# Optimization experiments

Hardware: AMD Instinct MI355X
Metric: run time of the kernel (lower is better)

Reference implementation:

```python
import jax, jax.numpy as jnp
import numpy as np

S, B, H = 1024, 2, 1024
NH, NKV, HD = 16, 4, 64
E, TOPK, F = 8, 2, 2048
EPS = 1e-5


def _layer_norm(x, w, b):
    mu = jnp.mean(x, axis=-1, keepdims=True)
    var = jnp.mean(jnp.square(x - mu), axis=-1, keepdims=True)
    return (x - mu) * jax.lax.rsqrt(var + EPS) * w + b


def setup_inputs() -> dict:
    key = jax.random.key(0)
    ks = jax.random.split(key, 8)
    return {
        "hidden_states": jax.random.normal(ks[0], (S, B, H), jnp.float32),
        "ln1_weight": jnp.ones((H,), jnp.float32),
        "ln1_bias": jnp.zeros((H,), jnp.float32),
        "ln2_weight": jnp.ones((H,), jnp.float32),
        "ln2_bias": jnp.zeros((H,), jnp.float32),
        "qkv_weight": jax.random.normal(ks[1], ((NH + 2 * NKV) * HD, H), jnp.float32) * 0.02,
        "proj_weight": jax.random.normal(ks[2], (H, H), jnp.float32) * 0.02,
        "router_weight": jax.random.normal(ks[3], (E, H), jnp.float32) * 0.02,
        "moe_w1": jax.random.normal(ks[4], (E, H, F), jnp.float32) * 0.02,
        "moe_w2": jax.random.normal(ks[5], (E, F, H), jnp.float32) * 0.02,
    }


def reference(hidden_states, ln1_weight, ln1_bias, ln2_weight, ln2_bias,
              qkv_weight, proj_weight, router_weight, moe_w1, moe_w2):
    dtype = hidden_states.dtype
    # LN1 -> QKV projection
    ln1_out = _layer_norm(hidden_states, ln1_weight, ln1_bias)            # [S,B,H]
    qkv = jnp.einsum('sbh,oh->sbo', ln1_out, qkv_weight)                  # [S,B,(NH+2NKV)*HD]
    q = qkv[..., : NH * HD].reshape(S, B, NH, HD)
    k = qkv[..., NH * HD: (NH + NKV) * HD].reshape(S, B, NKV, HD)
    v = qkv[..., (NH + NKV) * HD:].reshape(S, B, NKV, HD)
    # GQA: expand kv heads (repeat_interleave along head dim)
    ratio = NH // NKV
    k = jnp.repeat(k, ratio, axis=2)                                      # [S,B,NH,HD]
    v = jnp.repeat(v, ratio, axis=2)
    # [S,B,h,d] -> [B,h,S,d]
    qb = jnp.transpose(q, (1, 2, 0, 3))
    kb = jnp.transpose(k, (1, 2, 0, 3))
    vb = jnp.transpose(v, (1, 2, 0, 3))
    scale = 1.0 / np.sqrt(HD)
    scores = jnp.einsum('bhqd,bhkd->bhqk', qb, kb) * scale                # [B,NH,S,S]
    causal = jnp.tril(jnp.ones((S, S), bool))
    scores = jnp.where(causal, scores, jnp.finfo(dtype).min)
    attn = jax.nn.softmax(scores, axis=-1)
    attn_out = jnp.einsum('bhqk,bhkd->bhqd', attn, vb)                    # [B,NH,S,HD]
    attn_out = jnp.transpose(attn_out, (2, 0, 1, 3)).reshape(S, B, H)     # [S,B,H]
    proj_out = jnp.einsum('sbh,oh->sbo', attn_out, proj_weight)
    hidden_after_attn = hidden_states + proj_out
    # LN2 -> MoE
    ln2_flat = _layer_norm(hidden_after_attn, ln2_weight, ln2_bias).reshape(-1, H)  # [T,H]
    logits = jnp.einsum('th,eh->te', ln2_flat, router_weight)             # [T,E]
    probs = jax.nn.softmax(logits, axis=-1)
    top_probs, top_idx = jax.lax.top_k(probs, TOPK)                       # [T,K]
    # combine gate: sum_k prob_k * onehot(expert_k)  -> [T,E]
    gate = jnp.sum(jax.nn.one_hot(top_idx, E, dtype=dtype) * top_probs[..., None], axis=1)
    # dense all-expert grouped GEMM equivalent of dispatch/FC1/act/FC2/combine
    h1 = jnp.einsum('th,ehf->tef', ln2_flat, moe_w1)                      # [T,E,F]
    a1 = jax.nn.gelu(h1)
    y = jnp.einsum('tef,efh->teh', a1, moe_w2)                            # [T,E,H]
    moe_out = jnp.einsum('te,teh->th', gate, y).reshape(S, B, H)
    return hidden_after_attn + moe_out
```

## Files before the change

### kernel.cpp

```cpp
#include <hip/hip_runtime.h>
#include <hip/hip_bf16.h>

typedef unsigned short u16;
typedef __attribute__((ext_vector_type(8))) short s16x8;
typedef __attribute__((ext_vector_type(4))) short s16x4;
typedef __attribute__((ext_vector_type(4))) float f32x4;

#define SEQ 1024
#define BATCH 2
#define HID 1024
#define NHEAD 16
#define NKVH 4
#define HDIM 64
#define NEXP 8
#define FFN 2048
#define TOK (SEQ*BATCH)
#define QKVO ((NHEAD + 2*NKVH)*HDIM)
#define NPART 80
#define PREC 2112

#define GL16(gp, lp) __builtin_amdgcn_global_load_lds( \
    (const __attribute__((address_space(1))) unsigned int*)(gp), \
    (__attribute__((address_space(3))) unsigned int*)(lp), 16, 0, 0)

#define WAVE_LDS_FENCE() do { \
    asm volatile("s_waitcnt lgkmcnt(0)" ::: "memory"); \
    __builtin_amdgcn_sched_barrier(0); \
} while (0)

__device__ __forceinline__ float b2f(u16 u) {
    unsigned int x = ((unsigned int)u) << 16;
    return __uint_as_float(x);
}
__device__ __forceinline__ u16 f2b(float f) {
    unsigned int x = __float_as_uint(f);
    x = (x + 0x7FFFu + ((x >> 16) & 1u)) >> 16;
    return (u16)x;
}
__device__ __forceinline__ void split2(float x, u16& hi, u16& lo) {
    hi = f2b(x);
    lo = f2b(x - b2f(hi));
}
__device__ __forceinline__ f32x4 mfma16(s16x8 a, s16x8 b, f32x4 c) {
    return __builtin_amdgcn_mfma_f32_16x16x32_bf16(a, b, c, 0, 0, 0);
}
__device__ __forceinline__ float gelu_t(float x) {
    float x3 = x * x * x;
    return 0.5f * x * (1.0f + tanhf(0.7978845608028654f * (x + 0.044715f * x3)));
}

template<int OUTMODE>
__global__ __launch_bounds__(256) void ln_k(const float* __restrict__ xin,
    const float* __restrict__ wgt, const float* __restrict__ bia,
    float* __restrict__ outf, u16* __restrict__ outh, u16* __restrict__ outl)
{
    __shared__ float red[8];
    const int t = blockIdx.x, tid = threadIdx.x;
    f32x4 u = *((const f32x4*)(xin + (size_t)t * HID) + tid);
    float s = u[0] + u[1] + u[2] + u[3];
    #pragma unroll
    for (int off = 32; off >= 1; off >>= 1) s += __shfl_xor(s, off);
    if ((tid & 63) == 0) red[tid >> 6] = s;
    __syncthreads();
    float mu = (red[0] + red[1] + red[2] + red[3]) * (1.0f / HID);
    float d0 = u[0]-mu, d1 = u[1]-mu, d2 = u[2]-mu, d3 = u[3]-mu;
    float ss = d0*d0 + d1*d1 + d2*d2 + d3*d3;
    #pragma unroll
    for (int off = 32; off >= 1; off >>= 1) ss += __shfl_xor(ss, off);
    if ((tid & 63) == 0) red[4 + (tid >> 6)] = ss;
    __syncthreads();
    float var = (red[4] + red[5] + red[6] + red[7]) * (1.0f / HID);
    float rs = 1.0f / sqrtf(var + 1e-5f);
    f32x4 wv = *((const f32x4*)wgt + tid);
    f32x4 bv = *((const f32x4*)bia + tid);
    f32x4 o;
    o[0] = d0*rs*wv[0] + bv[0];
    o[1] = d1*rs*wv[1] + bv[1];
    o[2] = d2*rs*wv[2] + bv[2];
    o[3] = d3*rs*wv[3] + bv[3];
    if (OUTMODE == 0 || OUTMODE >= 3)
        *((f32x4*)(outf + (size_t)t * HID) + tid) = o;
    if (OUTMODE == 2 || OUTMODE == 3) {
        s16x4 h, l;
        #pragma unroll
        for (int j = 0; j < 4; ++j) {
            u16 hb, lb; split2(o[j], hb, lb);
            h[j] = (short)hb; l[j] = (short)lb;
        }
        *((s16x4*)(outh + (size_t)t * HID) + tid) = h;
        *((s16x4*)(outl + (size_t)t * HID) + tid) = l;
    }
    if (OUTMODE == 4) {
        s16x4 h;
        #pragma unroll
        for (int j = 0; j < 4; ++j) h[j] = (short)f2b(o[j]);
        *((s16x4*)(outh + (size_t)t * HID) + tid) = h;
    }
}

__global__ __launch_bounds__(256) void split_cast2_k(
    const float* __restrict__ inA, u16* __restrict__ hiA, u16* __restrict__ loA, int nA4,
    const float* __restrict__ inB, u16* __restrict__ hiB, u16* __restrict__ loB)
{
    int i = blockIdx.x * 256 + threadIdx.x;
    const float* in; u16* hi; u16* lo;
    if (i < nA4) { in = inA; hi = hiA; lo = loA; }
    else { i -= nA4; in = inB; hi = hiB; lo = loB; }
    f32x4 v = ((const f32x4*)in)[i];
    s16x4 h, l;
    #pragma unroll
    for (int j = 0; j < 4; ++j) {
        u16 hb, lb; split2(v[j], hb, lb);
        h[j] = (short)hb; l[j] = (short)lb;
    }
    ((s16x4*)hi)[i] = h;
    ((s16x4*)lo)[i] = l;
}

__global__ __launch_bounds__(256) void trans_cast_k(const float* __restrict__ in,
    u16* __restrict__ out, int R, int C)
{
    __shared__ float tile[64][65];
    const int e = blockIdx.z;
    const float* src = in + (size_t)e * R * C;
    u16* dst = out + (size_t)e * C * R;
    const int r0 = blockIdx.y * 64, c0 = blockIdx.x * 64;
    const int tr = threadIdx.x >> 2, tc = (threadIdx.x & 3) * 16;
    #pragma unroll
    for (int j = 0; j < 4; ++j) {
        f32x4 v = *(const f32x4*)(src + (size_t)(r0 + tr) * C + c0 + tc + j * 4);
        *(f32x4*)&tile[tr][tc + j * 4] = v;
    }
    __syncthreads();
    s16x8 o0, o1;
    #pragma unroll
    for (int j = 0; j < 8; ++j) o0[j] = (short)f2b(tile[tc + j][tr]);
    #pragma unroll
    for (int j = 0; j < 8; ++j) o1[j] = (short)f2b(tile[tc + 8 + j][tr]);
    u16* dp = dst + (size_t)(c0 + tr) * R + r0 + tc;
    *(s16x8*)dp = o0;
    *(s16x8*)(dp + 8) = o1;
}

template<int AMODE, int TERMS, int EPI, int TILE, int KU>
__global__ __launch_bounds__(256, 2) void gemm_db(
    const u16* __restrict__ Ah, const u16* __restrict__ Al,
    const u16* __restrict__ Bh, const u16* __restrict__ Bl,
    void* __restrict__ Cv, const float* __restrict__ RES, float* __restrict__ C2,
    const int* __restrict__ glist, const int* __restrict__ offs,
    const int* __restrict__ cnts, const float* __restrict__ slot_p,
    int M, int N, int K, int lda, int ldb, int ldc, long long bStrideE, int nx)
{
    constexpr int BM = (TILE == 2) ? 64 : 128;
    constexpr int BN = (TILE == 0) ? 128 : 64;
    constexpr int MI = (TILE == 0) ? 4 : ((TILE == 1) ? 2 : 1);
    constexpr bool A2 = (BM == 128);
    constexpr bool B2 = (BN == 128);
    __shared__ u16 AHs[2][KU][BM][32];
    __shared__ u16 ALs[(TERMS >= 2) ? 2 : 1][(TERMS >= 2) ? KU : 1][(TERMS >= 2) ? BM : 1][32];
    __shared__ u16 BHs[2][KU][BN][32];
    __shared__ u16 BLs[(TERMS >= 3) ? 2 : 1][(TERMS >= 3) ? KU : 1][(TERMS >= 3) ? BN : 1][32];

    const int tid = threadIdx.x;
    int m0, n0;
    int off = 0, cnt = M;
    if (AMODE == 0) {
        const int bid = blockIdx.x;
        const int xcd = bid & 7, j = bid >> 3;
        const int npx = nx >> 3;
        n0 = (xcd * npx + j % npx) * BN;
        m0 = (j / npx) * BM;
    } else {
        const int e = blockIdx.z;
        n0 = blockIdx.x * BN;
        m0 = blockIdx.y * BM;
        off = offs[e]; cnt = cnts[e];
        if (m0 >= cnt) return;
        long long be = (long long)e * bStrideE;
        Bh += be;
        if (TERMS >= 3) Bl += be;
    }
    const int lane = tid & 63, w = tid >> 6;
    const int wmB = (TILE == 0) ? ((w >> 1) * 64) : (w * (BM / 4));
    const int wnB = (TILE == 0) ? ((w & 1) * 64) : 0;
    const int l16 = lane & 15, grp = lane >> 4;
    const int srow = lane >> 2, schk = (lane & 3) * 8;
    const int lrA = w * (BM / 4);
    const int lrB = w * (BN / 4);

    long long ga0, ga1 = 0;
    {
        int am0 = m0 + lrA + srow;
        int am1 = am0 + 16;
        long long r0, r1;
        if (AMODE == 0) { r0 = am0; r1 = am1; }
        else if (AMODE == 1) {
            r0 = glist[off + ((am0 < cnt) ? am0 : 0)];
            r1 = A2 ? glist[off + ((am1 < cnt) ? am1 : 0)] : 0;
        } else {
            r0 = off + ((am0 < cnt) ? am0 : 0);
            r1 = A2 ? (off + ((am1 < cnt) ? am1 : 0)) : 0;
        }
        ga0 = r0 * lda + schk;
        if (A2) ga1 = r1 * lda + schk;
    }
    const long long gb0 = (long long)(n0 + lrB + srow) * ldb + schk;
    const long long gb1 = gb0 + 16LL * ldb;

    auto stage = [&](int bf, int k0) {
        #pragma unroll
        for (int u = 0; u < KU; ++u) {
            const int ko = k0 + u * 32;
            GL16(Ah + ga0 + ko, &AHs[bf][u][lrA][0]);
            if constexpr (A2) GL16(Ah + ga1 + ko, &AHs[bf][u][lrA + 16][0]);
            if constexpr (TERMS >= 2) {
                GL16(Al + ga0 + ko, &ALs[bf][u][lrA][0]);
                if constexpr (A2) GL16(Al + ga1 + ko, &ALs[bf][u][lrA + 16][0]);
            }
            GL16(Bh + gb0 + ko, &BHs[bf][u][lrB][0]);
            if constexpr (B2) GL16(Bh + gb1 + ko, &BHs[bf][u][lrB + 16][0]);
            if constexpr (TERMS >= 3) {
                GL16(Bl + gb0 + ko, &BLs[bf][u][lrB][0]);
                if constexpr (B2) GL16(Bl + gb1 + ko, &BLs[bf][u][lrB + 16][0]);
            }
        }
    };

    f32x4 acc[MI][4];
    #pragma unroll
    for (int i = 0; i < MI; ++i)
        #pragma unroll
        for (int j = 0; j < 4; ++j) acc[i][j] = f32x4{0.f, 0.f, 0.f, 0.f};

    const int nk = K / (32 * KU);
    int cur = 0;
    stage(0, 0);
    __syncthreads();
    for (int t = 0; t < nk; ++t) {
        if (t + 1 < nk) stage(cur ^ 1, (t + 1) * 32 * KU);
        #pragma unroll
        for (int u = 0; u < KU; ++u) {
            s16x8 ah[MI], al[MI], bh[4], bl[4];
            #pragma unroll
            for (int i = 0; i < MI; ++i)
                ah[i] = *(const s16x8*)&AHs[cur][u][wmB + i * 16 + l16][grp * 8];
            if constexpr (TERMS >= 2) {
                #pragma unroll
                for (int i = 0; i < MI; ++i)
                    al[i] = *(const s16x8*)&ALs[cur][u][wmB + i * 16 + l16][grp * 8];
            }
            #pragma unroll
            for (int j = 0; j < 4; ++j)
                bh[j] = *(const s16x8*)&BHs[cur][u][wnB + j * 16 + l16][grp * 8];
            if constexpr (TERMS >= 3) {
                #pragma unroll
                for (int j = 0; j < 4; ++j)
                    bl[j] = *(const s16x8*)&BLs[cur][u][wnB + j * 16 + l16][grp * 8];
            }
            #pragma unroll
            for (int i = 0; i < MI; ++i) {
                #pragma unroll
                for (int j = 0; j < 4; ++j) {
                    acc[i][j] = mfma16(ah[i], bh[j], acc[i][j]);
                    if constexpr (TERMS >= 3) acc[i][j] = mfma16(ah[i], bl[j], acc[i][j]);
                    if constexpr (TERMS >= 2) acc[i][j] = mfma16(al[i], bh[j], acc[i][j]);
                }
            }
        }
        __syncthreads();
        cur ^= 1;
    }
    #pragma unroll
    for (int i = 0; i < MI; ++i) {
        #pragma unroll
        for (int j = 0; j < 4; ++j) {
            int col = n0 + wnB + j * 16 + l16;
            #pragma unroll
            for (int r = 0; r < 4; ++r) {
                int mr = m0 + wmB + i * 16 + grp * 4 + r;
                if (AMODE != 0 && mr >= cnt) continue;
                long long crow = (AMODE == 0) ? mr : (off + mr);
                float val = acc[i][j][r];
                if (EPI == 0) {
                    ((float*)Cv)[crow * ldc + col] = val;
                } else if (EPI == 1) {
                    ((float*)Cv)[crow * ldc + col] = val + RES[crow * ldc + col];
                } else if (EPI == 2) {
                    ((u16*)Cv)[crow * ldc + col] = f2b(gelu_t(val));
                } else if (EPI == 5) {
                    ((u16*)Cv)[crow * ldc + col] = f2b(val);
                } else {
                    float v2 = val + RES[crow * ldc + col];
                    ((float*)Cv)[crow * ldc + col] = v2;
                    C2[crow * ldc + col] = v2;
                }
            }
        }
    }
}

__global__ __launch_bounds__(256) void kvprep(const float* __restrict__ qkvf,
    u16* __restrict__ kTh, u16* __restrict__ kTl,
    u16* __restrict__ vTh, u16* __restrict__ vTl)
{
    __shared__ float tile[64][68];
    const int st = blockIdx.x * 64;
    const int b = blockIdx.y & 1, kvh = blockIdx.y >> 1;
    const int tid = threadIdx.x;
    #pragma unroll
    for (int h = 0; h < 4; ++h) {
        int c = tid + h * 256;
        int srow = c >> 4, dseg = c & 15;
        f32x4 v = *(const f32x4*)(qkvf + (size_t)((st + srow) * BATCH + b) * QKVO
                                  + (NHEAD + NKVH) * HDIM + kvh * HDIM + dseg * 4);
        *(f32x4*)&tile[srow][dseg * 4] = v;
    }
    {
        int row = tid >> 2, qseg = tid & 3;
        const float* kr = qkvf + (size_t)((st + row) * BATCH + b) * QKVO
                          + NHEAD * HDIM + kvh * HDIM + qseg * 16;
        size_t ko = ((size_t)((b * NKVH + kvh) * SEQ + st + row)) * HDIM + qseg * 16;
        #pragma unroll
        for (int c = 0; c < 4; ++c) {
            f32x4 x = *(const f32x4*)(kr + c * 4);
            s16x4 vh, vl;
            #pragma unroll
            for (int j = 0; j < 4; ++j) {
                u16 hb, lb; split2(x[j], hb, lb);
                vh[j] = (short)hb; vl[j] = (short)lb;
            }
            *(s16x4*)(kTh + ko + c * 4) = vh;
            *(s16x4*)(kTl + ko + c * 4) = vl;
        }
    }
    __syncthreads();
    #pragma unroll
    for (int h = 0; h < 2; ++h) {
        int c = tid + h * 256;
        int drow = c >> 3, sseg = c & 7;
        s16x8 vh, vl;
        #pragma unroll
        for (int j = 0; j < 8; ++j) {
            u16 hb, lb; split2(tile[sseg * 8 + j][drow], hb, lb);
            vh[j] = (short)hb; vl[j] = (short)lb;
        }
        size_t oo = ((size_t)((b * NKVH + kvh) * HDIM + drow)) * SEQ + st + sseg * 8;
        *(s16x8*)(vTh + oo) = vh;
        *(s16x8*)(vTl + oo) = vl;
    }
}

__global__ __launch_bounds__(64, 3) void attn_part(
    const float* __restrict__ qkvf,
    const u16* __restrict__ kTh, const u16* __restrict__ kTl,
    const u16* __restrict__ vTh, const u16* __restrict__ vTl,
    float* __restrict__ part)
{
    __shared__ u16 plh[32][40];
    __shared__ u16 pll[32][40];
    const int p = blockIdx.x;
    int qt, c;
    if (p < 32)      { c = 0; qt = p; }
    else if (p < 56) { c = 1; qt = p - 24; }
    else if (p < 72) { c = 2; qt = p - 40; }
    else             { c = 3; qt = p - 48; }
    const int h = blockIdx.y, b = blockIdx.z;
    const int kvh = h >> 2;
    const int lane = threadIdx.x, l16 = lane & 15, grp = lane >> 4;

    const short one_bf16 = (short)0x3F80;
    const s16x8 ones = {one_bf16, one_bf16, one_bf16, one_bf16,
                        one_bf16, one_bf16, one_bf16, one_bf16};

    s16x8 qh[2][2], ql[2][2];
    #pragma unroll
    for (int mt = 0; mt < 2; ++mt) {
        const float* qb = qkvf + (size_t)((qt * 32 + mt * 16 + l16) * BATCH + b) * QKVO
                          + h * HDIM + grp * 8;
        #pragma unroll
        for (int ks = 0; ks < 2; ++ks) {
            f32x4 x0 = *(const f32x4*)(qb + ks * 32);
            f32x4 x1 = *(const f32x4*)(qb + ks * 32 + 4);
            #pragma unroll
            for (int j = 0; j < 4; ++j) {
                u16 hb, lb;
                split2(x0[j], hb, lb);
                qh[mt][ks][j] = (short)hb; ql[mt][ks][j] = (short)lb;
                split2(x1[j], hb, lb);
                qh[mt][ks][4 + j] = (short)hb; ql[mt][ks][4 + j] = (short)lb;
            }
        }
    }
    float mrow[2][4];
    f32x4 lsum[2];
    f32x4 o[2][4];
    #pragma unroll
    for (int mt = 0; mt < 2; ++mt) {
        #pragma unroll
        for (int r = 0; r < 4; ++r) mrow[mt][r] = -__builtin_inff();
        lsum[mt] = f32x4{0.f, 0.f, 0.f, 0.f};
        #pragma unroll
        for (int db = 0; db < 4; ++db) o[mt][db] = f32x4{0.f, 0.f, 0.f, 0.f};
    }

    const size_t kvbase = (size_t)(b * NKVH + kvh) * SEQ;
    const int kv0 = c * 256;
    const int kv_hi = min(kv0 + 256, qt * 32 + 32);
    const int nt = (kv_hi - kv0 + 31) >> 5;
    for (int jb = 0; jb < nt; ++jb) {
        const int kvb = kv0 + jb * 32;
        f32x4 s[2][2];
        #pragma unroll
        for (int t2 = 0; t2 < 2; ++t2) {
            size_t kb = (kvbase + kvb + t2 * 16 + l16) * HDIM + grp * 8;
            f32x4 z0 = f32x4{0.f, 0.f, 0.f, 0.f};
            f32x4 z1 = f32x4{0.f, 0.f, 0.f, 0.f};
            #pragma unroll
            for (int ks = 0; ks < 2; ++ks) {
                s16x8 kh = *(const s16x8*)(kTh + kb + ks * 32);
                s16x8 kl = *(const s16x8*)(kTl + kb + ks * 32);
                z0 = mfma16(qh[0][ks], kh, z0);
                z0 = mfma16(qh[0][ks], kl, z0);
                z0 = mfma16(ql[0][ks], kh, z0);
                z1 = mfma16(qh[1][ks], kh, z1);
                z1 = mfma16(qh[1][ks], kl, z1);
                z1 = mfma16(ql[1][ks], kh, z1);
            }
            s[0][t2] = z0; s[1][t2] = z1;
        }
        #pragma unroll
        for (int mt = 0; mt < 2; ++mt) {
            #pragma unroll
            for (int r = 0; r < 4; ++r) {
                const int qrow = qt * 32 + mt * 16 + grp * 4 + r;
                float a0 = s[mt][0][r] * 0.125f; if (kvb + l16 > qrow) a0 = -__builtin_inff();
                float a1 = s[mt][1][r] * 0.125f; if (kvb + 16 + l16 > qrow) a1 = -__builtin_inff();
                float mx = fmaxf(a0, a1);
                #pragma unroll
                for (int t = 1; t < 16; t <<= 1) mx = fmaxf(mx, __shfl_xor(mx, t));
                float mn = fmaxf(mrow[mt][r], mx);
                float sc = __expf(mrow[mt][r] - mn);
                mrow[mt][r] = mn;
                s[mt][0][r] = __expf(a0 - mn);
                s[mt][1][r] = __expf(a1 - mn);
                lsum[mt][r] *= sc;
                #pragma unroll
                for (int db = 0; db < 4; ++db) o[mt][db][r] *= sc;
            }
        }
        WAVE_LDS_FENCE();
        #pragma unroll
        for (int mt = 0; mt < 2; ++mt) {
            #pragma unroll
            for (int t2 = 0; t2 < 2; ++t2) {
                #pragma unroll
                for (int r = 0; r < 4; ++r) {
                    u16 hb, lb; split2(s[mt][t2][r], hb, lb);
                    plh[mt * 16 + grp * 4 + r][t2 * 16 + l16] = hb;
                    pll[mt * 16 + grp * 4 + r][t2 * 16 + l16] = lb;
                }
            }
        }
        WAVE_LDS_FENCE();
        s16x8 pah0 = *(const s16x8*)&plh[l16][grp * 8];
        s16x8 pal0 = *(const s16x8*)&pll[l16][grp * 8];
        s16x8 pah1 = *(const s16x8*)&plh[16 + l16][grp * 8];
        s16x8 pal1 = *(const s16x8*)&pll[16 + l16][grp * 8];
        lsum[0] = mfma16(pah0, ones, lsum[0]);
        lsum[0] = mfma16(pal0, ones, lsum[0]);
        lsum[1] = mfma16(pah1, ones, lsum[1]);
        lsum[1] = mfma16(pal1, ones, lsum[1]);
        #pragma unroll
        for (int db = 0; db < 4; ++db) {
            size_t vo = ((size_t)((b * NKVH + kvh) * HDIM + db * 16 + l16)) * SEQ + kvb + grp * 8;
            s16x8 vh = *(const s16x8*)(vTh + vo);
            s16x8 vl = *(const s16x8*)(vTl + vo);
            o[0][db] = mfma16(pah0, vh, o[0][db]);
            o[0][db] = mfma16(pah0, vl, o[0][db]);
            o[0][db] = mfma16(pal0, vh, o[0][db]);
            o[1][db] = mfma16(pah1, vh, o[1][db]);
            o[1][db] = mfma16(pah1, vl, o[1][db]);
            o[1][db] = mfma16(pal1, vh, o[1][db]);
        }
    }
    float* rec = part + (((size_t)(b * NHEAD + h) * NPART + p) * PREC);
    #pragma unroll
    for (int mt = 0; mt < 2; ++mt) {
        #pragma unroll
        for (int db = 0; db < 4; ++db) {
            #pragma unroll
            for (int r = 0; r < 4; ++r)
                rec[(mt * 16 + grp * 4 + r) * 64 + db * 16 + l16] = o[mt][db][r];
        }
    }
    if (l16 == 0) {
        #pragma unroll
        for (int mt = 0; mt < 2; ++mt) {
            #pragma unroll
            for (int r = 0; r < 4; ++r) {
                rec[2048 + mt * 16 + grp * 4 + r] = mrow[mt][r];
                rec[2080 + mt * 16 + grp * 4 + r] = lsum[mt][r];
            }
        }
    }
}

__global__ __launch_bounds__(256) void attn_comb(const float* __restrict__ part,
    u16* __restrict__ attn_h, u16* __restrict__ attn_l)
{
    const int qt16 = blockIdx.x, h = blockIdx.y, b = blockIdx.z;
    const int qt32 = qt16 >> 1;
    const int lrow = (qt16 & 1) * 16 + (threadIdx.x >> 4);
    const int nch = (qt32 >> 3) + 1;
    const int c4 = (threadIdx.x & 15) * 4;
    const size_t base = (size_t)(b * NHEAD + h) * NPART;
    const int pbase[4] = {0, 24, 40, 48};
    float mv[4], lv[4];
    float M = -__builtin_inff();
    #pragma unroll
    for (int c = 0; c < 4; ++c) {
        if (c < nch) {
            const float* rec = part + (base + pbase[c] + qt32) * PREC;
            mv[c] = rec[2048 + lrow];
            lv[c] = rec[2080 + lrow];
            M = fmaxf(M, mv[c]);
        }
    }
    float L = 0.f;
    f32x4 acc = f32x4{0.f, 0.f, 0.f, 0.f};
    #pragma unroll
    for (int c = 0; c < 4; ++c) {
        if (c < nch) {
            const float* rec = part + (base + pbase[c] + qt32) * PREC;
            float wgt = __expf(mv[c] - M);
            L += lv[c] * wgt;
            f32x4 ov = *(const f32x4*)(rec + lrow * 64 + c4);
            acc[0] += ov[0] * wgt; acc[1] += ov[1] * wgt;
            acc[2] += ov[2] * wgt; acc[3] += ov[3] * wgt;
        }
    }
    float inv = 1.f / L;
    const int qrow = qt32 * 32 + lrow;
    size_t oo = (size_t)(qrow * BATCH + b) * HID + h * HDIM + c4;
    #pragma unroll
    for (int j = 0; j < 4; ++j) {
        u16 hb, lb; split2(acc[j] * inv, hb, lb);
        attn_h[oo + j] = hb;
        attn_l[oo + j] = lb;
    }
}

__global__ __launch_bounds__(64) void router_k(const float* __restrict__ ln2,
    const float* __restrict__ rw, int* __restrict__ e01, float* __restrict__ p01)
{
    const int t = blockIdx.x, lane = threadIdx.x;
    const float* xr = ln2 + (size_t)t * HID + lane * 16;
    float x[16];
    #pragma unroll
    for (int c = 0; c < 4; ++c) {
        f32x4 u = *(const f32x4*)(xr + c * 4);
        #pragma unroll
        for (int j = 0; j < 4; ++j) x[c * 4 + j] = u[j];
    }
    float lg[8];
    #pragma unroll
    for (int e = 0; e < 8; ++e) {
        const float* wr = rw + (size_t)e * HID + lane * 16;
        float a = 0.f;
        #pragma unroll
        for (int c = 0; c < 4; ++c) {
            f32x4 wv = *(const f32x4*)(wr + c * 4);
            #pragma unroll
            for (int j = 0; j < 4; ++j) a += x[c * 4 + j] * wv[j];
        }
        #pragma unroll
        for (int off = 32; off >= 1; off >>= 1) a += __shfl_xor(a, off);
        lg[e] = a;
    }
    float mx = lg[0];
    #pragma unroll
    for (int e = 1; e < 8; ++e) mx = fmaxf(mx, lg[e]);
    float pe[8], ssum = 0.f;
    #pragma unroll
    for (int e = 0; e < 8; ++e) { pe[e] = expf(lg[e] - mx); ssum += pe[e]; }
    float inv = 1.f / ssum;
    int e0 = 0; float b0 = -1.f;
    #pragma unroll
    for (int e = 0; e < 8; ++e) { float p = pe[e] * inv; if (p > b0) { b0 = p; e0 = e; } }
    int e1 = -1; float b1 = -1.f;
    #pragma unroll
    for (int e = 0; e < 8; ++e) {
        if (e == e0) continue;
        float p = pe[e] * inv; if (p > b1) { b1 = p; e1 = e; }
    }
    if (lane == 0) {
        e01[2 * t] = e0; e01[2 * t + 1] = e1;
        p01[2 * t] = b0; p01[2 * t + 1] = b1;
    }
}

__global__ __launch_bounds__(64) void scatter_det(const int* __restrict__ e01,
    const float* __restrict__ p01, int* __restrict__ cnt, int* __restrict__ offs,
    int* __restrict__ tok_of, float* __restrict__ slot_p, int* __restrict__ slot_of)
{
    const int e = blockIdx.x;
    const int lane = threadIdx.x;
    int myc[8] = {0, 0, 0, 0, 0, 0, 0, 0};
    for (int i = lane; i < 2 * TOK; i += 64) {
        int ei = e01[i];
        #pragma unroll
        for (int ee = 0; ee < 8; ++ee) myc[ee] += (ei == ee) ? 1 : 0;
    }
    #pragma unroll
    for (int ee = 0; ee < 8; ++ee) {
        int v = myc[ee];
        #pragma unroll
        for (int off = 32; off >= 1; off >>= 1) v += __shfl_xor(v, off);
        myc[ee] = v;
    }
    int base = 0;
    #pragma unroll
    for (int ee = 0; ee < 8; ++ee) if (ee < e) base += myc[ee];
    if (lane == 0) { cnt[e] = myc[e]; offs[e] = base; }
    for (int c = 0; c < TOK; c += 64) {
        int t = c + lane;
        int kk = -1;
        if (e01[2 * t] == e) kk = 0;
        else if (e01[2 * t + 1] == e) kk = 1;
        int f = (kk >= 0) ? 1 : 0;
        int sc = f;
        #pragma unroll
        for (int o = 1; o < 64; o <<= 1) {
            int nn = __shfl_up(sc, o);
            if (lane >= o) sc += nn;
        }
        if (kk >= 0) {
            int slot = base + sc - 1;
            tok_of[slot] = t;
            slot_p[slot] = p01[2 * t + kk];
            slot_of[2 * t + kk] = slot;
        }
        base += __shfl(sc, 63);
    }
}

__global__ __launch_bounds__(256) void moe_comb(const u16* __restrict__ yb,
    const int* __restrict__ slot_of, const float* __restrict__ p01,
    float* __restrict__ out)
{
    const int t = blockIdx.x;
    const int c4 = threadIdx.x * 4;
    const int s0 = slot_of[2 * t], s1 = slot_of[2 * t + 1];
    const float p0 = p01[2 * t], p1 = p01[2 * t + 1];
    s16x4 y0 = *(const s16x4*)(yb + (size_t)s0 * HID + c4);
    s16x4 y1 = *(const s16x4*)(yb + (size_t)s1 * HID + c4);
    f32x4 o = *(f32x4*)(out + (size_t)t * HID + c4);
    #pragma unroll
    for (int j = 0; j < 4; ++j)
        o[j] += p0 * b2f((u16)y0[j]) + p1 * b2f((u16)y1[j]);
    *(f32x4*)(out + (size_t)t * HID + c4) = o;
}

__global__ void sentinel_k(float* out) {
    out[blockIdx.x * 256 + threadIdx.x] = 12345.0f;
}

extern "C" void kernel_launch(void* const* d_in, const int* in_sizes, int n_in,
                              void* d_out, int out_size, void* d_ws, size_t ws_size,
                              hipStream_t stream)
{
    (void)in_sizes; (void)n_in; (void)out_size;
    const float* hs    = (const float*)d_in[0];
    const float* ln1w  = (const float*)d_in[1];
    const float* ln1b  = (const float*)d_in[2];
    const float* ln2w  = (const float*)d_in[3];
    const float* ln2b  = (const float*)d_in[4];
    const float* qkvw  = (const float*)d_in[5];
    const float* projw = (const float*)d_in[6];
    const float* rw    = (const float*)d_in[7];
    const float* w1    = (const float*)d_in[8];
    const float* w2    = (const float*)d_in[9];
    float* out = (float*)d_out;
    char* ws = (char*)d_ws;

    size_t o = 0;
    auto alloc = [&](size_t bytes) -> void* {
        void* p = ws + o; o += (bytes + 255) & ~(size_t)255; return p;
    };
    u16*   w1t    = (u16*)alloc((size_t)NEXP * FFN * HID * 2);
    u16*   w2t    = (u16*)alloc((size_t)NEXP * HID * FFN * 2);
    u16*   qkvwh  = (u16*)alloc((size_t)QKVO * HID * 2);
    u16*   qkvwl  = (u16*)alloc((size_t)QKVO * HID * 2);
    u16*   projwh = (u16*)alloc((size_t)HID * HID * 2);
    u16*   projwl = (u16*)alloc((size_t)HID * HID * 2);
    u16*   ln1h   = (u16*)alloc((size_t)TOK * HID * 2);
    u16*   ln1l   = (u16*)alloc((size_t)TOK * HID * 2);
    float* qkvf   = (float*)alloc((size_t)TOK * QKVO * 4);
    u16*   kTh    = (u16*)alloc((size_t)BATCH * NKVH * SEQ * HDIM * 2);
    u16*   kTl    = (u16*)alloc((size_t)BATCH * NKVH * SEQ * HDIM * 2);
    u16*   vTh    = (u16*)alloc((size_t)BATCH * NKVH * HDIM * SEQ * 2);
    u16*   vTl    = (u16*)alloc((size_t)BATCH * NKVH * HDIM * SEQ * 2);
    float* haf    = (float*)alloc((size_t)TOK * HID * 4);
    u16*   ln2h   = (u16*)alloc((size_t)TOK * HID * 2);
    u16*   a1b    = (u16*)alloc((size_t)TOK * 2 * FFN * 2);
    int*   e01    = (int*)alloc(TOK * 2 * 4);
    float* p01    = (float*)alloc(TOK * 2 * 4);
    int*   cnt    = (int*)alloc(256);
    int*   offs   = (int*)alloc(256);
    int*   tok_of = (int*)alloc(TOK * 2 * 4);
    float* slot_p = (float*)alloc(TOK * 2 * 4);
    int*   slot_of = (int*)alloc(TOK * 2 * 4);
    size_t need = o;

    if (ws_size < need) {
        sentinel_k<<<TOK * HID / 256, 256, 0, stream>>>(out);
        return;
    }

    u16* attnh = ln1h;
    u16* attnl = ln1l;
    float* ln2f = qkvf;
    u16*  yb = (u16*)qkvf;
    float* part = (float*)w1t;

    split_cast2_k<<<(QKVO * HID + HID * HID) / 4 / 256, 256, 0, stream>>>(
        qkvw, qkvwh, qkvwl, QKVO * HID / 4, projw, projwh, projwl);
    ln_k<2><<<TOK, 256, 0, stream>>>(hs, ln1w, ln1b, nullptr, ln1h, ln1l);
    gemm_db<0, 3, 0, 2, 1><<<(QKVO / 64) * (TOK / 64), 256, 0, stream>>>(
        ln1h, ln1l, qkvwh, qkvwl, qkvf, nullptr, nullptr, nullptr, nullptr, nullptr, nullptr,
        TOK, QKVO, HID, HID, HID, QKVO, 0, QKVO / 64);
    kvprep<<<dim3(SEQ / 64, BATCH * NKVH), 256, 0, stream>>>(qkvf, kTh, kTl, vTh, vTl);
    attn_part<<<dim3(NPART, NHEAD, BATCH), 64, 0, stream>>>(
        qkvf, kTh, kTl, vTh, vTl, part);
    attn_comb<<<dim3(SEQ / 16, NHEAD, BATCH), 256, 0, stream>>>(part, attnh, attnl);
    gemm_db<0, 3, 4, 2, 1><<<(HID / 64) * (TOK / 64), 256, 0, stream>>>(
        attnh, attnl, projwh, projwl, haf, hs, out, nullptr, nullptr, nullptr, nullptr,
        TOK, HID, HID, HID, HID, HID, 0, HID / 64);
    ln_k<4><<<TOK, 256, 0, stream>>>(haf, ln2w, ln2b, ln2f, ln2h, nullptr);
    trans_cast_k<<<dim3(FFN / 64, HID / 64, NEXP), 256, 0, stream>>>(w1, w1t, HID, FFN);
    trans_cast_k<<<dim3(HID / 64, FFN / 64, NEXP), 256, 0, stream>>>(w2, w2t, FFN, HID);
    router_k<<<TOK, 64, 0, stream>>>(ln2f, rw, e01, p01);
    scatter_det<<<NEXP, 64, 0, stream>>>(e01, p01, cnt, offs, tok_of, slot_p, slot_of);
    gemm_db<1, 1, 2, 1, 2><<<dim3(FFN / 64, TOK / 128, NEXP), 256, 0, stream>>>(
        ln2h, nullptr, w1t, nullptr, a1b, nullptr, nullptr, tok_of, offs, cnt, nullptr,
        0, FFN, HID, HID, HID, FFN, (long long)FFN * HID, FFN / 64);
    gemm_db<2, 1, 5, 1, 2><<<dim3(HID / 64, TOK / 128, NEXP), 256, 0, stream>>>(
        a1b, nullptr, w2t, nullptr, yb, nullptr, nullptr, tok_of, offs, cnt, slot_p,
        0, HID, FFN, FFN, FFN, HID, (long long)HID * FFN, HID / 64);
    moe_comb<<<TOK, 256, 0, stream>>>(yb, slot_of, p01, out);
}
```

Measured before the change: 310.8 us.

## Add triple-buffered direct-to-LDS bf16 GEMM for MoE expert FC1/FC2

Adds a dedicated gemm_p3 kernel for the two grouped MoE expert GEMMs. It uses a three-stage LDS ring filled by global_load_lds, explicit vmcnt waits and a 128x64 tile with each wave owning 32 rows. It also sets launch_bounds occupancy 2 and drops the unused generic template paths. The aim is to hide global-load latency better than the previous double-buffered gemm_db, at the cost of more LDS per block and hand-tuned wait counts that must match the exact number of issued loads.

```diff
diff --git a/kernel.cpp b/kernel.cpp
--- a/kernel.cpp
+++ b/kernel.cpp
@@ -285,14 +285,119 @@
                     ((float*)Cv)[crow * ldc + col] = val;
                 } else if (EPI == 1) {
                     ((float*)Cv)[crow * ldc + col] = val + RES[crow * ldc + col];
-                } else if (EPI == 2) {
-                    ((u16*)Cv)[crow * ldc + col] = f2b(gelu_t(val));
-                } else if (EPI == 5) {
-                    ((u16*)Cv)[crow * ldc + col] = f2b(val);
                 } else {
                     float v2 = val + RES[crow * ldc + col];
                     ((float*)Cv)[crow * ldc + col] = v2;
                     C2[crow * ldc + col] = v2;
+                }
+            }
+        }
+    }
+}
+
+template<int AMODE, int EPI>
+__global__ __launch_bounds__(256, 2) void gemm_p3(
+    const u16* __restrict__ Ah, const u16* __restrict__ Bh, void* __restrict__ Cv,
+    const int* __restrict__ glist, const int* __restrict__ offs,
+    const int* __restrict__ cnts,
+    int M, int N, int K, int lda, int ldb, int ldc, long long bStrideE)
+{
+    constexpr int BM = 128, BN = 64, MI = 2;
+    __shared__ u16 AHs[3][BM][32];
+    __shared__ u16 BHs[3][BN][32];
+
+    const int tid = threadIdx.x;
+    const int e = blockIdx.z;
+    const int n0 = blockIdx.x * BN;
+    const int m0 = blockIdx.y * BM;
+    const int off = offs[e];
+    const int cnt = cnts[e];
+    if (m0 >= cnt) return;
+    const u16* B = Bh + (long long)e * bStrideE;
+
+    const int lane = tid & 63, w = tid >> 6;
+    const int wmB = w * 32;
+    const int l16 = lane & 15, grp = lane >> 4;
+    const int srow = lane >> 2, schk = (lane & 3) * 8;
+    const int lrA = w * 32;
+    const int lrB = w * 16;
+
+    long long ga0, ga1;
+    {
+        int am0 = m0 + lrA + srow;
+        int am1 = am0 + 16;
+        long long r0, r1;
+        if (AMODE == 1) {
+            r0 = glist[off + ((am0 < cnt) ? am0 : 0)];
+            r1 = glist[off + ((am1 < cnt) ? am1 : 0)];
+        } else {
+            r0 = off + ((am0 < cnt) ? am0 : 0);
+            r1 = off + ((am1 < cnt) ? am1 : 0);
+        }
+        ga0 = r0 * lda + schk;
+        ga1 = r1 * lda + schk;
+    }
+    const long long gb0 = (long long)(n0 + lrB + srow) * ldb + schk;
+
+    auto stage = [&](int bf, int k0) {
+        GL16(Ah + ga0 + k0, &AHs[bf][lrA][0]);
+        GL16(Ah + ga1 + k0, &AHs[bf][lrA + 16][0]);
+        GL16(B + gb0 + k0, &BHs[bf][lrB][0]);
+    };
+
+    f32x4 acc[MI][4];
+    #pragma unroll
+    for (int i = 0; i < MI; ++i)
+        #pragma unroll
+        for (int j = 0; j < 4; ++j) acc[i][j] = f32x4{0.f, 0.f, 0.f, 0.f};
+
+    const int nk = K >> 5;
+    stage(0, 0);
+    stage(1, 32);
+    for (int t = 0; t < nk; ++t) {
+        if (t + 2 < nk) stage((t + 2) % 3, (t + 2) * 32);
+        if (t + 2 < nk) {
+            asm volatile("s_waitcnt vmcnt(6)" ::: "memory");
+        } else if (t + 1 < nk) {
+            asm volatile("s_waitcnt vmcnt(3)" ::: "memory");
+        } else {
+            asm volatile("s_waitcnt vmcnt(0)" ::: "memory");
+        }
+        __builtin_amdgcn_sched_barrier(0);
+        __builtin_amdgcn_s_barrier();
+        const int buf = t % 3;
+        s16x8 ah[MI], bh[4];
+        #pragma unroll
+        for (int i = 0; i < MI; ++i)
+            ah[i] = *(const s16x8*)&AHs[buf][wmB + i * 16 + l16][grp * 8];
+        #pragma unroll
+        for (int j = 0; j < 4; ++j)
+            bh[j] = *(const s16x8*)&BHs[buf][lrB - lrB + j * 16 + l16][grp * 8];
+        #pragma unroll
+        for (int i = 0; i < MI; ++i) {
+            #pragma unroll
+            for (int j = 0; j < 4; ++j)
+                acc[i][j] = mfma16(ah[i], bh[j], acc[i][j]);
+        }
+        asm volatile("s_waitcnt lgkmcnt(0)" ::: "memory");
+        __builtin_amdgcn_sched_barrier(0);
+        __builtin_amdgcn_s_barrier();
+    }
+    #pragma unroll
+    for (int i = 0; i < MI; ++i) {
+        #pragma unroll
+        for (int j = 0; j < 4; ++j) {
+            int col = n0 + j * 16 + l16;
+            #pragma unroll
+            for (int r = 0; r < 4; ++r) {
+                int mr = m0 + wmB + i * 16 + grp * 4 + r;
+                if (mr >= cnt) continue;
+                long long crow = off + mr;
+                float val = acc[i][j][r];
+                if (EPI == 2) {
+                    ((u16*)Cv)[crow * ldc + col] = f2b(gelu_t(val));
+                } else {
+                    ((u16*)Cv)[crow * ldc + col] = f2b(val);
                 }
             }
         }
@@ -741,11 +846,11 @@
     trans_cast_k<<<dim3(HID / 64, FFN / 64, NEXP), 256, 0, stream>>>(w2, w2t, FFN, HID);
     router_k<<<TOK, 64, 0, stream>>>(ln2f, rw, e01, p01);
     scatter_det<<<NEXP, 64, 0, stream>>>(e01, p01, cnt, offs, tok_of, slot_p, slot_of);
-    gemm_db<1, 1, 2, 1, 2><<<dim3(FFN / 64, TOK / 128, NEXP), 256, 0, stream>>>(
-        ln2h, nullptr, w1t, nullptr, a1b, nullptr, nullptr, tok_of, offs, cnt, nullptr,
-        0, FFN, HID, HID, HID, FFN, (long long)FFN * HID, FFN / 64);
-    gemm_db<2, 1, 5, 1, 2><<<dim3(HID / 64, TOK / 128, NEXP), 256, 0, stream>>>(
-        a1b, nullptr, w2t, nullptr, yb, nullptr, nullptr, tok_of, offs, cnt, slot_p,
-        0, HID, FFN, FFN, FFN, HID, (long long)HID * FFN, HID / 64);
+    gemm_p3<1, 2><<<dim3(FFN / 64, TOK / 128, NEXP), 256, 0, stream>>>(
+        ln2h, w1t, a1b, tok_of, offs, cnt,
+        0, FFN, HID, HID, HID, FFN, (long long)FFN * HID);
+    gemm_p3<2, 5><<<dim3(HID / 64, TOK / 128, NEXP), 256, 0, stream>>>(
+        a1b, w2t, yb, tok_of, offs, cnt,
+        0, HID, FFN, FFN, FFN, HID, (long long)HID * FFN);
     moe_comb<<<TOK, 256, 0, stream>>>(yb, slot_of, p01, out);
 }
```

Result: slower. 327.1 us (+5.2%).

## Split-K the MoE FC2 grouped GEMM with atomic fp32 accumulation

Applied to the files above, without the earlier changes.

The second expert GEMM is split into two K halves, which doubles the grid along z, and each half atomically adds its partial result into a zeroed fp32 buffer. The combine kernel now reads fp32 instead of bf16. The aim is more blocks and better CU occupancy for the expert GEMM, which has few tiles per expert. In exchange it adds a zeroing kernel, atomic traffic, a larger fp32 intermediate, and a summation order that is not deterministic.

```diff
diff --git a/kernel.cpp b/kernel.cpp
--- a/kernel.cpp
+++ b/kernel.cpp
@@ -171,14 +171,18 @@
         n0 = (xcd * npx + j % npx) * BN;
         m0 = (j / npx) * BM;
     } else {
-        const int e = blockIdx.z;
+        const int zz = blockIdx.z;
+        const int e = zz & 7;
+        const int kof = (zz >> 3) * K;
         n0 = blockIdx.x * BN;
         m0 = blockIdx.y * BM;
         off = offs[e]; cnt = cnts[e];
         if (m0 >= cnt) return;
         long long be = (long long)e * bStrideE;
-        Bh += be;
-        if (TERMS >= 3) Bl += be;
+        Bh += be + kof;
+        Ah += kof;
+        if (TERMS >= 2) Al += kof;
+        if (TERMS >= 3) Bl += be + kof;
     }
     const int lane = tid & 63, w = tid >> 6;
     const int wmB = (TILE == 0) ? ((w >> 1) * 64) : (w * (BM / 4));
@@ -289,6 +293,8 @@
                     ((u16*)Cv)[crow * ldc + col] = f2b(gelu_t(val));
                 } else if (EPI == 5) {
                     ((u16*)Cv)[crow * ldc + col] = f2b(val);
+                } else if (EPI == 6) {
+                    atomicAdd((float*)Cv + crow * ldc + col, val);
                 } else {
                     float v2 = val + RES[crow * ldc + col];
                     ((float*)Cv)[crow * ldc + col] = v2;
@@ -644,7 +650,12 @@
     }
 }
 
-__global__ __launch_bounds__(256) void moe_comb(const u16* __restrict__ yb,
+__global__ __launch_bounds__(256) void zero_k(float* __restrict__ p)
+{
+    ((f32x4*)p)[blockIdx.x * 256 + threadIdx.x] = f32x4{0.f, 0.f, 0.f, 0.f};
+}
+
+__global__ __launch_bounds__(256) void moe_comb(const float* __restrict__ yf,
     const int* __restrict__ slot_of, const float* __restrict__ p01,
     float* __restrict__ out)
 {
@@ -652,12 +663,12 @@
     const int c4 = threadIdx.x * 4;
     const int s0 = slot_of[2 * t], s1 = slot_of[2 * t + 1];
     const float p0 = p01[2 * t], p1 = p01[2 * t + 1];
-    s16x4 y0 = *(const s16x4*)(yb + (size_t)s0 * HID + c4);
-    s16x4 y1 = *(const s16x4*)(yb + (size_t)s1 * HID + c4);
+    f32x4 y0 = *(const f32x4*)(yf + (size_t)s0 * HID + c4);
+    f32x4 y1 = *(const f32x4*)(yf + (size_t)s1 * HID + c4);
     f32x4 o = *(f32x4*)(out + (size_t)t * HID + c4);
     #pragma unroll
     for (int j = 0; j < 4; ++j)
-        o[j] += p0 * b2f((u16)y0[j]) + p1 * b2f((u16)y1[j]);
+        o[j] += p0 * y0[j] + p1 * y1[j];
     *(f32x4*)(out + (size_t)t * HID + c4) = o;
 }
 
@@ -720,7 +731,7 @@
     u16* attnh = ln1h;
     u16* attnl = ln1l;
     float* ln2f = qkvf;
-    u16*  yb = (u16*)qkvf;
+    float* yf = qkvf;
     float* part = (float*)w1t;
 
     split_cast2_k<<<(QKVO * HID + HID * HID) / 4 / 256, 256, 0, stream>>>(
@@ -744,8 +755,9 @@
     gemm_db<1, 1, 2, 1, 2><<<dim3(FFN / 64, TOK / 128, NEXP), 256, 0, stream>>>(
         ln2h, nullptr, w1t, nullptr, a1b, nullptr, nullptr, tok_of, offs, cnt, nullptr,
         0, FFN, HID, HID, HID, FFN, (long long)FFN * HID, FFN / 64);
-    gemm_db<2, 1, 5, 1, 2><<<dim3(HID / 64, TOK / 128, NEXP), 256, 0, stream>>>(
-        a1b, nullptr, w2t, nullptr, yb, nullptr, nullptr, tok_of, offs, cnt, slot_p,
-        0, HID, FFN, FFN, FFN, HID, (long long)HID * FFN, HID / 64);
-    moe_comb<<<TOK, 256, 0, stream>>>(yb, slot_of, p01, out);
-}
+    zero_k<<<TOK * 2 * HID / 4 / 256, 256, 0, stream>>>(yf);
+    gemm_db<2, 1, 6, 1, 2><<<dim3(HID / 64, TOK / 128, NEXP * 2), 256, 0, stream>>>(
+        a1b, nullptr, w2t, nullptr, yf, nullptr, nullptr, tok_of, offs, cnt, slot_p,
+        0, HID, FFN / 2, FFN, FFN, HID, (long long)HID * FFN, HID / 64);
+    moe_comb<<<TOK, 256, 0, stream>>>(yf, slot_of, p01, out);
+}
```

Result: slower. 322.9 us (+3.9%).
